# Kernel optimization log

Measured on AMD Instinct MI355X. Metric: run time of the kernel, lower is better.

The kernel has to match this reference:

```python
import jax, jax.numpy as jnp
import numpy as np

EPS = 1e-12
SIMILARITY = 'l2'


def setup_inputs() -> dict:
    key = jax.random.key(0)
    k1, k2, k3, k4 = jax.random.split(key, 4)
    N, M, D = 8192, 8192, 256
    x = jax.random.normal(k1, (N, D), dtype=jnp.float32)
    x_n = jax.random.normal(k2, (M, D), dtype=jnp.float32)
    W = jax.random.normal(k3, (D, 2), dtype=jnp.float32) / np.sqrt(D)
    b = jax.random.normal(k4, (2,), dtype=jnp.float32)
    return {"x": x, "x_n": x_n, "W": W, "b": b}


def _sim_matrix(x, x_n, similarity):
    if similarity == 'l2':
        x2 = jnp.sum(x * x, axis=1, keepdims=True)          # [N,1]
        xn2 = jnp.sum(x_n * x_n, axis=1, keepdims=True).T    # [1,M]
        d2 = jnp.maximum(x2 + xn2 - 2.0 * (x @ x_n.T), 0.0)
        return -jnp.sqrt(d2)
    elif similarity == 'l1':
        return -jnp.sum(jnp.abs(x[:, None, :] - x_n[None, :, :]), axis=-1)
    elif similarity == 'dot':
        return (x @ x_n.T) / x.shape[1]
    elif similarity == 'cos':
        xn_ = x / jnp.linalg.norm(x, axis=1, keepdims=True)
        xnn = x_n / jnp.linalg.norm(x_n, axis=1, keepdims=True)
        return xn_ @ xnn.T
    raise ValueError(similarity)


def reference(x, x_n, W, b) -> jnp.ndarray:
    # soft-KNN params from a small linear head
    params = jax.nn.sigmoid(x @ W + b)                      # [N,2]
    k = jnp.clip(params[:, 0:1], EPS, 1.0 - EPS)            # [N,1]
    t = jnp.clip(params[:, 1:2], EPS, 1.0 - EPS)            # [N,1]

    sim = _sim_matrix(x, x_n, SIMILARITY)                   # [N,M]
    sim_min = jnp.min(sim, axis=1, keepdims=True)
    sim_max = jnp.max(sim, axis=1, keepdims=True)
    sim = (sim - sim_min) / (sim_max - sim_min)             # row min-max normalize
    sim = jnp.maximum(sim, EPS)

    shift = t / (1.0 - t) * (k - sim) * jnp.log(sim / k)
    return sim + jnp.where(sim <= k, shift, 0.0)
```

## Files before the change

### kernel.cpp

```cpp
#include <hip/hip_runtime.h>
#include <hip/hip_bf16.h>
#include <cstdint>

#define N_ROWS 8192
#define M_ROWS 8192
#define DDIM   256
#define EPSF   1e-12f

typedef unsigned short u16;
typedef __attribute__((ext_vector_type(8))) short short8;
typedef __attribute__((ext_vector_type(4))) float floatx4;

__device__ inline void split_bf16(float v, u16& h, u16& lo) {
    __hip_bfloat16 hb = __float2bfloat16(v);
    float hf = __bfloat162float(hb);
    __hip_bfloat16 lb = __float2bfloat16(v - hf);
    h  = __builtin_bit_cast(u16, hb);
    lo = __builtin_bit_cast(u16, lb);
}

__global__ __launch_bounds__(256) void prep_x(
    const float* __restrict__ x, const float* __restrict__ W, const float* __restrict__ b,
    u16* __restrict__ xhi, u16* __restrict__ xlo,
    float* __restrict__ x2, float* __restrict__ karr, float* __restrict__ Carr,
    float* __restrict__ logkarr)
{
    const int l = threadIdx.x & 63;
    const int w = threadIdx.x >> 6;
    const int row = blockIdx.x * 4 + w;

    const float4 xv = *(const float4*)(x + (size_t)row * DDIM + l * 4);
    const float4 wa = *(const float4*)(W + l * 8);
    const float4 wb = *(const float4*)(W + l * 8 + 4);

    float s2 = xv.x * xv.x + xv.y * xv.y + xv.z * xv.z + xv.w * xv.w;
    float s0 = xv.x * wa.x + xv.y * wa.z + xv.z * wb.x + xv.w * wb.z;
    float s1 = xv.x * wa.y + xv.y * wa.w + xv.z * wb.y + xv.w * wb.w;

    u16 h0, l0, h1, l1, h2, l2, h3, l3;
    split_bf16(xv.x, h0, l0); split_bf16(xv.y, h1, l1);
    split_bf16(xv.z, h2, l2); split_bf16(xv.w, h3, l3);
    *(ushort4*)(xhi + (size_t)row * DDIM + l * 4) = make_ushort4(h0, h1, h2, h3);
    *(ushort4*)(xlo + (size_t)row * DDIM + l * 4) = make_ushort4(l0, l1, l2, l3);

    #pragma unroll
    for (int off = 32; off; off >>= 1) {
        s2 += __shfl_xor(s2, off);
        s0 += __shfl_xor(s0, off);
        s1 += __shfl_xor(s1, off);
    }
    if (l == 0) {
        float a0 = s0 + b[0];
        float a1 = s1 + b[1];
        float k = 1.0f / (1.0f + __expf(-a0));
        float t = 1.0f / (1.0f + __expf(-a1));
        k = fminf(fmaxf(k, EPSF), 1.0f - EPSF);
        t = fminf(fmaxf(t, EPSF), 1.0f - EPSF);
        x2[row] = s2;
        karr[row] = k;
        Carr[row] = t / (1.0f - t);
        logkarr[row] = logf(k);
    }
}

__global__ __launch_bounds__(256) void prep_xn(
    const float* __restrict__ xn,
    u16* __restrict__ xnhi, u16* __restrict__ xnlo, float* __restrict__ xn2)
{
    const int l = threadIdx.x & 63;
    const int w = threadIdx.x >> 6;
    const int row = blockIdx.x * 4 + w;

    const float4 xv = *(const float4*)(xn + (size_t)row * DDIM + l * 4);
    float s2 = xv.x * xv.x + xv.y * xv.y + xv.z * xv.z + xv.w * xv.w;

    u16 h0, l0, h1, l1, h2, l2, h3, l3;
    split_bf16(xv.x, h0, l0); split_bf16(xv.y, h1, l1);
    split_bf16(xv.z, h2, l2); split_bf16(xv.w, h3, l3);
    *(ushort4*)(xnhi + (size_t)row * DDIM + l * 4) = make_ushort4(h0, h1, h2, h3);
    *(ushort4*)(xnlo + (size_t)row * DDIM + l * 4) = make_ushort4(l0, l1, l2, l3);

    #pragma unroll
    for (int off = 32; off; off >>= 1) s2 += __shfl_xor(s2, off);
    if (l == 0) xn2[row] = s2;
}

__global__ __launch_bounds__(256) void gemm_s(
    const u16* __restrict__ xhi, const u16* __restrict__ xlo,
    const u16* __restrict__ xnhi, const u16* __restrict__ xnlo,
    const float* __restrict__ x2, const float* __restrict__ xn2,
    float* __restrict__ out)
{
    __shared__ u16 lds[16384];

    const int l  = threadIdx.x & 63;
    const int w  = threadIdx.x >> 6;
    const int wm = w >> 1;
    const int wn = w & 1;
    const int bRow = blockIdx.y;
    const int bCol = blockIdx.x;

    floatx4 acc[4][4];
    #pragma unroll
    for (int mi = 0; mi < 4; ++mi)
        #pragma unroll
        for (int ni = 0; ni < 4; ++ni)
            acc[mi][ni] = (floatx4){0.f, 0.f, 0.f, 0.f};

    const u16* bases[4] = {xhi, xlo, xnhi, xnlo};
    const int lrow = l & 15;
    const int lk8  = (l >> 4) * 8;

    for (int kk = 0; kk < DDIM / 32; ++kk) {
        const int ks = kk * 32;
        #pragma unroll
        for (int p = 0; p < 8; ++p) {
            const int id    = w * 8 + p;
            const int panel = id >> 3;
            const int tile  = id & 7;
            const int grow  = (panel < 2 ? bRow : bCol) * 128 + tile * 16 + lrow;
            const u16* src  = bases[panel] + (size_t)grow * DDIM + ks + lk8;
            u16* dst = &lds[panel * 4096 + tile * 512];
            __builtin_amdgcn_global_load_lds(
                (const __attribute__((address_space(1))) void*)src,
                (__attribute__((address_space(3))) void*)dst,
                16, 0, 0);
        }
        __syncthreads();

        short8 ah[4], al[4], bh[4], bl[4];
        #pragma unroll
        for (int i = 0; i < 4; ++i) {
            ah[i] = *(const short8*)&lds[0     + (wm * 4 + i) * 512 + l * 8];
            al[i] = *(const short8*)&lds[4096  + (wm * 4 + i) * 512 + l * 8];
            bh[i] = *(const short8*)&lds[8192  + (wn * 4 + i) * 512 + l * 8];
            bl[i] = *(const short8*)&lds[12288 + (wn * 4 + i) * 512 + l * 8];
        }
        #pragma unroll
        for (int mi = 0; mi < 4; ++mi)
            #pragma unroll
            for (int ni = 0; ni < 4; ++ni) {
                acc[mi][ni] = __builtin_amdgcn_mfma_f32_16x16x32_bf16(ah[mi], bh[ni], acc[mi][ni], 0, 0, 0);
                acc[mi][ni] = __builtin_amdgcn_mfma_f32_16x16x32_bf16(ah[mi], bl[ni], acc[mi][ni], 0, 0, 0);
                acc[mi][ni] = __builtin_amdgcn_mfma_f32_16x16x32_bf16(al[mi], bh[ni], acc[mi][ni], 0, 0, 0);
            }
        __syncthreads();
    }

    const int q  = l >> 4;
    const int cn = l & 15;
    #pragma unroll
    for (int mi = 0; mi < 4; ++mi) {
        #pragma unroll
        for (int r = 0; r < 4; ++r) {
            const int i = bRow * 128 + wm * 64 + mi * 16 + q * 4 + r;
            const float x2i = x2[i];
            #pragma unroll
            for (int ni = 0; ni < 4; ++ni) {
                const int j = bCol * 128 + wn * 64 + ni * 16 + cn;
                const float d2 = x2i + xn2[j] - 2.0f * acc[mi][ni][r];
                out[(size_t)i * M_ROWS + j] = -sqrtf(fmaxf(d2, 0.0f));
            }
        }
    }
}

__global__ __launch_bounds__(256) void transform_row(
    float* __restrict__ out, const float* __restrict__ x, const float* __restrict__ xn,
    const float* __restrict__ karr, const float* __restrict__ Carr,
    const float* __restrict__ logkarr)
{
    const int row = blockIdx.x;
    const int t = threadIdx.x;
    const int l = t & 63;
    const int w = t >> 6;

    __shared__ float wmin[4], wmax[4];
    __shared__ int cnt;
    __shared__ unsigned long long sMinBits;
    __shared__ int cidx[1024];
    __shared__ double cval[1024];

    const size_t rbase = (size_t)row * M_ROWS;
    float4 v[8];
    #pragma unroll
    for (int c = 0; c < 8; ++c)
        v[c] = *(const float4*)(out + rbase + c * 1024 + t * 4);

    float lmin = 1e30f, lmax = -1e30f;
    #pragma unroll
    for (int c = 0; c < 8; ++c) {
        lmin = fminf(lmin, fminf(fminf(v[c].x, v[c].y), fminf(v[c].z, v[c].w)));
        lmax = fmaxf(lmax, fmaxf(fmaxf(v[c].x, v[c].y), fmaxf(v[c].z, v[c].w)));
    }
    #pragma unroll
    for (int m = 1; m < 64; m <<= 1) {
        lmin = fminf(lmin, __shfl_xor(lmin, m));
        lmax = fmaxf(lmax, __shfl_xor(lmax, m));
    }
    if (l == 0) { wmin[w] = lmin; wmax[w] = lmax; }
    if (t == 0) { cnt = 0; sMinBits = 0ull; }
    __syncthreads();
    const float sminA = fminf(fminf(wmin[0], wmin[1]), fminf(wmin[2], wmin[3]));
    const float smaxA = fmaxf(fmaxf(wmax[0], wmax[1]), fmaxf(wmax[2], wmax[3]));
    const float thresh = sminA + 0.05f * (smaxA - sminA);

    int myPos[8], mySlot[8];
    int myCnt = 0;
    #pragma unroll
    for (int c = 0; c < 8; ++c) {
        const float* pv = (const float*)&v[c];
        #pragma unroll
        for (int u = 0; u < 4; ++u) {
            if (pv[u] <= thresh) {
                int pos = atomicAdd(&cnt, 1);
                if (pos < 1024 && myCnt < 8) {
                    cidx[pos] = c * 1024 + t * 4 + u;
                    myPos[myCnt] = pos;
                    mySlot[myCnt] = c * 4 + u;
                    myCnt++;
                }
            }
        }
    }
    __syncthreads();
    const int nc = min(cnt, 1024);

    const float4 xa = *(const float4*)(x + (size_t)row * DDIM + l * 4);
    const double dx0 = xa.x, dx1 = xa.y, dx2 = xa.z, dx3 = xa.w;
    double x2p = dx0 * dx0 + dx1 * dx1 + dx2 * dx2 + dx3 * dx3;
    #pragma unroll
    for (int m = 1; m < 64; m <<= 1) x2p += __shfl_xor(x2p, m);

    for (int c = w; c < nc; c += 4) {
        const int j = cidx[c];
        const float4 na = *(const float4*)(xn + (size_t)j * DDIM + l * 4);
        const double n0 = na.x, n1 = na.y, n2 = na.z, n3 = na.w;
        double dot = dx0 * n0 + dx1 * n1 + dx2 * n2 + dx3 * n3;
        double nn  = n0 * n0 + n1 * n1 + n2 * n2 + n3 * n3;
        #pragma unroll
        for (int m = 1; m < 64; m <<= 1) {
            dot += __shfl_xor(dot, m);
            nn  += __shfl_xor(nn, m);
        }
        if (l == 0) {
            double d2 = x2p + nn - 2.0 * dot;
            d2 = d2 > 0.0 ? d2 : 0.0;
            double se = -sqrt(d2);
            cval[c] = se;
            atomicMax(&sMinBits, (unsigned long long)__double_as_longlong(se));
        }
    }
    __syncthreads();

    const double sminD = __longlong_as_double((long long)sMinBits);
    const float k = karr[row], C = Carr[row], logk = logkarr[row];
    const float smin = (float)sminD;
    const double invD = 1.0 / ((double)smaxA - sminD);
    const float inv = (float)invD;

    float o[32];
    #pragma unroll
    for (int c = 0; c < 8; ++c) {
        const float* pv = (const float*)&v[c];
        #pragma unroll
        for (int u = 0; u < 4; ++u) {
            float sim = fmaxf((pv[u] - smin) * inv, EPSF);
            float r = sim;
            if (sim <= k) r += C * (k - sim) * (__logf(sim) - logk);
            o[c * 4 + u] = r;
        }
    }
    for (int q2 = 0; q2 < myCnt; ++q2) {
        double simd = (cval[myPos[q2]] - sminD) * invD;
        simd = simd > (double)EPSF ? simd : (double)EPSF;
        float sim = (float)simd;
        float r = sim;
        if (sim <= k) r += C * (k - sim) * (logf(sim) - logk);
        o[mySlot[q2]] = r;
    }
    #pragma unroll
    for (int c = 0; c < 8; ++c) {
        float4 ov;
        ov.x = o[c * 4 + 0]; ov.y = o[c * 4 + 1];
        ov.z = o[c * 4 + 2]; ov.w = o[c * 4 + 3];
        *(float4*)(out + rbase + c * 1024 + t * 4) = ov;
    }
}

extern "C" void kernel_launch(void* const* d_in, const int* in_sizes, int n_in,
                              void* d_out, int out_size, void* d_ws, size_t ws_size,
                              hipStream_t stream)
{
    const float* x  = (const float*)d_in[0];
    const float* xn = (const float*)d_in[1];
    const float* W  = (const float*)d_in[2];
    const float* b  = (const float*)d_in[3];
    float* out = (float*)d_out;

    uint8_t* ws = (uint8_t*)d_ws;
    u16* xhi  = (u16*)(ws);
    u16* xlo  = (u16*)(ws + (4u << 20));
    u16* xnhi = (u16*)(ws + (8u << 20));
    u16* xnlo = (u16*)(ws + (12u << 20));
    float* x2       = (float*)(ws + (16u << 20));
    float* xn2      = x2 + N_ROWS;
    float* karr     = xn2 + M_ROWS;
    float* Carr     = karr + N_ROWS;
    float* logkarr  = Carr + N_ROWS;

    prep_x<<<N_ROWS / 4, 256, 0, stream>>>(x, W, b, xhi, xlo, x2, karr, Carr, logkarr);
    prep_xn<<<M_ROWS / 4, 256, 0, stream>>>(xn, xnhi, xnlo, xn2);
    gemm_s<<<dim3(M_ROWS / 128, N_ROWS / 128), 256, 0, stream>>>(
        xhi, xlo, xnhi, xnlo, x2, xn2, out);
    transform_row<<<N_ROWS, 256, 0, stream>>>(out, x, xn, karr, Carr, logkarr);
}
```

Baseline: 519.2 us.

## Recompute single-bf16 GEMM twice to fuse transform and drop intermediate matrix

Replaces the 3-pass split-bf16 GEMM plus row-transform pass with two single-bf16 GEMM passes. The first pass only reduces per-row min/max distances via atomics, and the second recomputes the dot products and writes the final transformed output directly with nontemporal stores. Near-min candidates are collected into a global list, refined in double precision, and patched afterwards. This avoids writing and rereading the 256 MB similarity matrix and cuts MFMA work per pass, at the cost of a duplicated GEMM, lower bf16 accuracy elsewhere in each row, global atomic contention, and a capped candidate buffer.

New measurement: 1.166 ms. 124% more time.

```diff
diff --git a/kernel.cpp b/kernel.cpp
--- a/kernel.cpp
+++ b/kernel.cpp
@@ -6,24 +6,18 @@
 #define M_ROWS 8192
 #define DDIM   256
 #define EPSF   1e-12f
+#define CAND_CAP (1 << 18)
+#define THRESH_FRAC 0.08f
 
 typedef unsigned short u16;
+typedef unsigned long long u64;
 typedef __attribute__((ext_vector_type(8))) short short8;
 typedef __attribute__((ext_vector_type(4))) float floatx4;
 
-__device__ inline void split_bf16(float v, u16& h, u16& lo) {
-    __hip_bfloat16 hb = __float2bfloat16(v);
-    float hf = __bfloat162float(hb);
-    __hip_bfloat16 lb = __float2bfloat16(v - hf);
-    h  = __builtin_bit_cast(u16, hb);
-    lo = __builtin_bit_cast(u16, lb);
-}
-
 __global__ __launch_bounds__(256) void prep_x(
     const float* __restrict__ x, const float* __restrict__ W, const float* __restrict__ b,
-    u16* __restrict__ xhi, u16* __restrict__ xlo,
-    float* __restrict__ x2, float* __restrict__ karr, float* __restrict__ Carr,
-    float* __restrict__ logkarr)
+    u16* __restrict__ xhi, float* __restrict__ x2, float4* __restrict__ rowQ,
+    unsigned* __restrict__ rowD2MinU, unsigned* __restrict__ rowD2MaxU)
 {
     const int l = threadIdx.x & 63;
     const int w = threadIdx.x >> 6;
@@ -37,11 +31,12 @@
     float s0 = xv.x * wa.x + xv.y * wa.z + xv.z * wb.x + xv.w * wb.z;
     float s1 = xv.x * wa.y + xv.y * wa.w + xv.z * wb.y + xv.w * wb.w;
 
-    u16 h0, l0, h1, l1, h2, l2, h3, l3;
-    split_bf16(xv.x, h0, l0); split_bf16(xv.y, h1, l1);
-    split_bf16(xv.z, h2, l2); split_bf16(xv.w, h3, l3);
-    *(ushort4*)(xhi + (size_t)row * DDIM + l * 4) = make_ushort4(h0, h1, h2, h3);
-    *(ushort4*)(xlo + (size_t)row * DDIM + l * 4) = make_ushort4(l0, l1, l2, l3);
+    ushort4 hv;
+    hv.x = __builtin_bit_cast(u16, __float2bfloat16(xv.x));
+    hv.y = __builtin_bit_cast(u16, __float2bfloat16(xv.y));
+    hv.z = __builtin_bit_cast(u16, __float2bfloat16(xv.z));
+    hv.w = __builtin_bit_cast(u16, __float2bfloat16(xv.w));
+    *(ushort4*)(xhi + (size_t)row * DDIM + l * 4) = hv;
 
     #pragma unroll
     for (int off = 32; off; off >>= 1) {
@@ -57,15 +52,14 @@
         k = fminf(fmaxf(k, EPSF), 1.0f - EPSF);
         t = fminf(fmaxf(t, EPSF), 1.0f - EPSF);
         x2[row] = s2;
-        karr[row] = k;
-        Carr[row] = t / (1.0f - t);
-        logkarr[row] = logf(k);
+        rowQ[row] = make_float4(k, t / (1.0f - t), logf(k), 0.0f);
+        rowD2MinU[row] = 0x7F7FFFFFu;
+        rowD2MaxU[row] = 0u;
     }
 }
 
 __global__ __launch_bounds__(256) void prep_xn(
-    const float* __restrict__ xn,
-    u16* __restrict__ xnhi, u16* __restrict__ xnlo, float* __restrict__ xn2)
+    const float* __restrict__ xn, u16* __restrict__ xnhi, float* __restrict__ xn2)
 {
     const int l = threadIdx.x & 63;
     const int w = threadIdx.x >> 6;
@@ -74,25 +68,69 @@
     const float4 xv = *(const float4*)(xn + (size_t)row * DDIM + l * 4);
     float s2 = xv.x * xv.x + xv.y * xv.y + xv.z * xv.z + xv.w * xv.w;
 
-    u16 h0, l0, h1, l1, h2, l2, h3, l3;
-    split_bf16(xv.x, h0, l0); split_bf16(xv.y, h1, l1);
-    split_bf16(xv.z, h2, l2); split_bf16(xv.w, h3, l3);
-    *(ushort4*)(xnhi + (size_t)row * DDIM + l * 4) = make_ushort4(h0, h1, h2, h3);
-    *(ushort4*)(xnlo + (size_t)row * DDIM + l * 4) = make_ushort4(l0, l1, l2, l3);
+    ushort4 hv;
+    hv.x = __builtin_bit_cast(u16, __float2bfloat16(xv.x));
+    hv.y = __builtin_bit_cast(u16, __float2bfloat16(xv.y));
+    hv.z = __builtin_bit_cast(u16, __float2bfloat16(xv.z));
+    hv.w = __builtin_bit_cast(u16, __float2bfloat16(xv.w));
+    *(ushort4*)(xnhi + (size_t)row * DDIM + l * 4) = hv;
 
     #pragma unroll
     for (int off = 32; off; off >>= 1) s2 += __shfl_xor(s2, off);
     if (l == 0) xn2[row] = s2;
 }
 
-__global__ __launch_bounds__(256) void gemm_s(
-    const u16* __restrict__ xhi, const u16* __restrict__ xlo,
-    const u16* __restrict__ xnhi, const u16* __restrict__ xnlo,
+__device__ __forceinline__ void gemm_core(
+    const u16* __restrict__ xhi, const u16* __restrict__ xnhi,
+    u16* lds, int bRow, int bCol, int l, int w, int wm, int wn,
+    floatx4 acc[4][4])
+{
+    const int lrow = l & 15;
+    const int lk8  = (l >> 4) * 8;
+    #pragma unroll
+    for (int mi = 0; mi < 4; ++mi)
+        #pragma unroll
+        for (int ni = 0; ni < 4; ++ni)
+            acc[mi][ni] = (floatx4){0.f, 0.f, 0.f, 0.f};
+
+    for (int kk = 0; kk < DDIM / 32; ++kk) {
+        const int ks = kk * 32;
+        #pragma unroll
+        for (int p = 0; p < 4; ++p) {
+            const int id    = w * 4 + p;
+            const int panel = id >> 3;
+            const int tile  = id & 7;
+            const int grow  = (panel == 0 ? bRow : bCol) * 128 + tile * 16 + lrow;
+            const u16* src  = (panel == 0 ? xhi : xnhi) + (size_t)grow * DDIM + ks + lk8;
+            u16* dst = &lds[panel * 4096 + tile * 512];
+            __builtin_amdgcn_global_load_lds(
+                (const __attribute__((address_space(1))) void*)src,
+                (__attribute__((address_space(3))) void*)dst,
+                16, 0, 0);
+        }
+        __syncthreads();
+
+        short8 ah[4], bh[4];
+        #pragma unroll
+        for (int i = 0; i < 4; ++i) {
+            ah[i] = *(const short8*)&lds[0    + (wm * 4 + i) * 512 + l * 8];
+            bh[i] = *(const short8*)&lds[4096 + (wn * 4 + i) * 512 + l * 8];
+        }
+        #pragma unroll
+        for (int mi = 0; mi < 4; ++mi)
+            #pragma unroll
+            for (int ni = 0; ni < 4; ++ni)
+                acc[mi][ni] = __builtin_amdgcn_mfma_f32_16x16x32_bf16(ah[mi], bh[ni], acc[mi][ni], 0, 0, 0);
+        __syncthreads();
+    }
+}
+
+__global__ __launch_bounds__(256) void gemm_minmax(
+    const u16* __restrict__ xhi, const u16* __restrict__ xnhi,
     const float* __restrict__ x2, const float* __restrict__ xn2,
-    float* __restrict__ out)
-{
-    __shared__ u16 lds[16384];
-
+    unsigned* __restrict__ rowD2MinU, unsigned* __restrict__ rowD2MaxU)
+{
+    __shared__ u16 lds[8192];
     const int l  = threadIdx.x & 63;
     const int w  = threadIdx.x >> 6;
     const int wm = w >> 1;
@@ -101,51 +139,7 @@
     const int bCol = blockIdx.x;
 
     floatx4 acc[4][4];
-    #pragma unroll
-    for (int mi = 0; mi < 4; ++mi)
-        #pragma unroll
-        for (int ni = 0; ni < 4; ++ni)
-            acc[mi][ni] = (floatx4){0.f, 0.f, 0.f, 0.f};
-
-    const u16* bases[4] = {xhi, xlo, xnhi, xnlo};
-    const int lrow = l & 15;
-    const int lk8  = (l >> 4) * 8;
-
-    for (int kk = 0; kk < DDIM / 32; ++kk) {
-        const int ks = kk * 32;
-        #pragma unroll
-        for (int p = 0; p < 8; ++p) {
-            const int id    = w * 8 + p;
-            const int panel = id >> 3;
-            const int tile  = id & 7;
-            const int grow  = (panel < 2 ? bRow : bCol) * 128 + tile * 16 + lrow;
-            const u16* src  = bases[panel] + (size_t)grow * DDIM + ks + lk8;
-            u16* dst = &lds[panel * 4096 + tile * 512];
-            __builtin_amdgcn_global_load_lds(
-                (const __attribute__((address_space(1))) void*)src,
-                (__attribute__((address_space(3))) void*)dst,
-                16, 0, 0);
-        }
-        __syncthreads();
-
-        short8 ah[4], al[4], bh[4], bl[4];
-        #pragma unroll
-        for (int i = 0; i < 4; ++i) {
-            ah[i] = *(const short8*)&lds[0     + (wm * 4 + i) * 512 + l * 8];
-            al[i] = *(const short8*)&lds[4096  + (wm * 4 + i) * 512 + l * 8];
-            bh[i] = *(const short8*)&lds[8192  + (wn * 4 + i) * 512 + l * 8];
-            bl[i] = *(const short8*)&lds[12288 + (wn * 4 + i) * 512 + l * 8];
-        }
-        #pragma unroll
-        for (int mi = 0; mi < 4; ++mi)
-            #pragma unroll
-            for (int ni = 0; ni < 4; ++ni) {
-                acc[mi][ni] = __builtin_amdgcn_mfma_f32_16x16x32_bf16(ah[mi], bh[ni], acc[mi][ni], 0, 0, 0);
-                acc[mi][ni] = __builtin_amdgcn_mfma_f32_16x16x32_bf16(ah[mi], bl[ni], acc[mi][ni], 0, 0, 0);
-                acc[mi][ni] = __builtin_amdgcn_mfma_f32_16x16x32_bf16(al[mi], bh[ni], acc[mi][ni], 0, 0, 0);
-            }
-        __syncthreads();
-    }
+    gemm_core(xhi, xnhi, lds, bRow, bCol, l, w, wm, wn, acc);
 
     const int q  = l >> 4;
     const int cn = l & 15;
@@ -155,136 +149,144 @@
         for (int r = 0; r < 4; ++r) {
             const int i = bRow * 128 + wm * 64 + mi * 16 + q * 4 + r;
             const float x2i = x2[i];
+            float dmn = 3.0e38f, dmx = 0.0f;
             #pragma unroll
             for (int ni = 0; ni < 4; ++ni) {
                 const int j = bCol * 128 + wn * 64 + ni * 16 + cn;
-                const float d2 = x2i + xn2[j] - 2.0f * acc[mi][ni][r];
-                out[(size_t)i * M_ROWS + j] = -sqrtf(fmaxf(d2, 0.0f));
+                const float d2 = fmaxf(x2i + xn2[j] - 2.0f * acc[mi][ni][r], 0.0f);
+                dmn = fminf(dmn, d2);
+                dmx = fmaxf(dmx, d2);
             }
-        }
-    }
-}
-
-__global__ __launch_bounds__(256) void transform_row(
-    float* __restrict__ out, const float* __restrict__ x, const float* __restrict__ xn,
-    const float* __restrict__ karr, const float* __restrict__ Carr,
-    const float* __restrict__ logkarr)
-{
-    const int row = blockIdx.x;
-    const int t = threadIdx.x;
-    const int l = t & 63;
-    const int w = t >> 6;
-
-    __shared__ float wmin[4], wmax[4];
-    __shared__ int cnt;
-    __shared__ unsigned long long sMinBits;
-    __shared__ int cidx[1024];
-    __shared__ double cval[1024];
-
-    const size_t rbase = (size_t)row * M_ROWS;
-    float4 v[8];
-    #pragma unroll
-    for (int c = 0; c < 8; ++c)
-        v[c] = *(const float4*)(out + rbase + c * 1024 + t * 4);
-
-    float lmin = 1e30f, lmax = -1e30f;
-    #pragma unroll
-    for (int c = 0; c < 8; ++c) {
-        lmin = fminf(lmin, fminf(fminf(v[c].x, v[c].y), fminf(v[c].z, v[c].w)));
-        lmax = fmaxf(lmax, fmaxf(fmaxf(v[c].x, v[c].y), fmaxf(v[c].z, v[c].w)));
-    }
-    #pragma unroll
-    for (int m = 1; m < 64; m <<= 1) {
-        lmin = fminf(lmin, __shfl_xor(lmin, m));
-        lmax = fmaxf(lmax, __shfl_xor(lmax, m));
-    }
-    if (l == 0) { wmin[w] = lmin; wmax[w] = lmax; }
-    if (t == 0) { cnt = 0; sMinBits = 0ull; }
-    __syncthreads();
-    const float sminA = fminf(fminf(wmin[0], wmin[1]), fminf(wmin[2], wmin[3]));
-    const float smaxA = fmaxf(fmaxf(wmax[0], wmax[1]), fmaxf(wmax[2], wmax[3]));
-    const float thresh = sminA + 0.05f * (smaxA - sminA);
-
-    int myPos[8], mySlot[8];
-    int myCnt = 0;
-    #pragma unroll
-    for (int c = 0; c < 8; ++c) {
-        const float* pv = (const float*)&v[c];
-        #pragma unroll
-        for (int u = 0; u < 4; ++u) {
-            if (pv[u] <= thresh) {
-                int pos = atomicAdd(&cnt, 1);
-                if (pos < 1024 && myCnt < 8) {
-                    cidx[pos] = c * 1024 + t * 4 + u;
-                    myPos[myCnt] = pos;
-                    mySlot[myCnt] = c * 4 + u;
-                    myCnt++;
+            #pragma unroll
+            for (int m = 1; m < 16; m <<= 1) {
+                dmn = fminf(dmn, __shfl_xor(dmn, m));
+                dmx = fmaxf(dmx, __shfl_xor(dmx, m));
+            }
+            if (cn == 0) {
+                atomicMin(&rowD2MinU[i], __float_as_uint(dmn));
+                atomicMax(&rowD2MaxU[i], __float_as_uint(dmx));
+            }
+        }
+    }
+}
+
+__global__ __launch_bounds__(256) void rowfin(
+    const unsigned* __restrict__ rowD2MinU, const unsigned* __restrict__ rowD2MaxU,
+    float4* __restrict__ rowP, u64* __restrict__ rowMinBits, int* __restrict__ cntG)
+{
+    const int i = blockIdx.x * 256 + threadIdx.x;
+    const float smax = -sqrtf(__uint_as_float(rowD2MinU[i]));
+    const float smin = -sqrtf(__uint_as_float(rowD2MaxU[i]));
+    const float range = smax - smin;
+    rowP[i] = make_float4(smin, 1.0f / range, smin + THRESH_FRAC * range, smax);
+    rowMinBits[i] = 0ull;
+    if (i == 0) *cntG = 0;
+}
+
+__global__ __launch_bounds__(256) void gemm_out(
+    const u16* __restrict__ xhi, const u16* __restrict__ xnhi,
+    const float* __restrict__ x2, const float* __restrict__ xn2,
+    const float4* __restrict__ rowP, const float4* __restrict__ rowQ,
+    float* __restrict__ out, unsigned* __restrict__ cand, int* __restrict__ cntG)
+{
+    __shared__ u16 lds[8192];
+    const int l  = threadIdx.x & 63;
+    const int w  = threadIdx.x >> 6;
+    const int wm = w >> 1;
+    const int wn = w & 1;
+    const int bRow = blockIdx.y;
+    const int bCol = blockIdx.x;
+
+    floatx4 acc[4][4];
+    gemm_core(xhi, xnhi, lds, bRow, bCol, l, w, wm, wn, acc);
+
+    const int q  = l >> 4;
+    const int cn = l & 15;
+    #pragma unroll
+    for (int mi = 0; mi < 4; ++mi) {
+        #pragma unroll
+        for (int r = 0; r < 4; ++r) {
+            const int i = bRow * 128 + wm * 64 + mi * 16 + q * 4 + r;
+            const float x2i  = x2[i];
+            const float4 P = rowP[i];
+            const float4 Q = rowQ[i];
+            #pragma unroll
+            for (int ni = 0; ni < 4; ++ni) {
+                const int j = bCol * 128 + wn * 64 + ni * 16 + cn;
+                const float d2 = fmaxf(x2i + xn2[j] - 2.0f * acc[mi][ni][r], 0.0f);
+                const float s = -sqrtf(d2);
+                if (s <= P.z) {
+                    int pos = atomicAdd(cntG, 1);
+                    if (pos < CAND_CAP) cand[pos] = ((unsigned)i << 13) | (unsigned)j;
                 }
+                float sim = fmaxf((s - P.x) * P.y, EPSF);
+                float rv = sim;
+                if (sim <= Q.x) rv += Q.y * (Q.x - sim) * (__logf(sim) - Q.z);
+                __builtin_nontemporal_store(rv, &out[(size_t)i * M_ROWS + j]);
             }
         }
     }
-    __syncthreads();
-    const int nc = min(cnt, 1024);
-
-    const float4 xa = *(const float4*)(x + (size_t)row * DDIM + l * 4);
-    const double dx0 = xa.x, dx1 = xa.y, dx2 = xa.z, dx3 = xa.w;
-    double x2p = dx0 * dx0 + dx1 * dx1 + dx2 * dx2 + dx3 * dx3;
-    #pragma unroll
-    for (int m = 1; m < 64; m <<= 1) x2p += __shfl_xor(x2p, m);
-
-    for (int c = w; c < nc; c += 4) {
-        const int j = cidx[c];
-        const float4 na = *(const float4*)(xn + (size_t)j * DDIM + l * 4);
-        const double n0 = na.x, n1 = na.y, n2 = na.z, n3 = na.w;
-        double dot = dx0 * n0 + dx1 * n1 + dx2 * n2 + dx3 * n3;
-        double nn  = n0 * n0 + n1 * n1 + n2 * n2 + n3 * n3;
+}
+
+__global__ __launch_bounds__(256) void refine(
+    const float* __restrict__ x, const float* __restrict__ xn,
+    const unsigned* __restrict__ cand, const int* __restrict__ cntG,
+    double* __restrict__ cexact, u64* __restrict__ rowMinBits)
+{
+    const int l = threadIdx.x & 63;
+    const int w = threadIdx.x >> 6;
+    const int gw = blockIdx.x * 4 + w;
+    const int nwaves = gridDim.x * 4;
+    const int nc = min(*cntG, CAND_CAP);
+
+    for (int c = gw; c < nc; c += nwaves) {
+        const unsigned rc = cand[c];
+        const int row = rc >> 13;
+        const int col = rc & 8191;
+        const float4 xa = *(const float4*)(x  + (size_t)row * DDIM + l * 4);
+        const float4 na = *(const float4*)(xn + (size_t)col * DDIM + l * 4);
+        const double x0 = xa.x, x1 = xa.y, x2v = xa.z, x3 = xa.w;
+        const double n0 = na.x, n1 = na.y, n2v = na.z, n3 = na.w;
+        double xx  = x0 * x0 + x1 * x1 + x2v * x2v + x3 * x3;
+        double nn  = n0 * n0 + n1 * n1 + n2v * n2v + n3 * n3;
+        double dot = x0 * n0 + x1 * n1 + x2v * n2v + x3 * n3;
         #pragma unroll
         for (int m = 1; m < 64; m <<= 1) {
+            xx  += __shfl_xor(xx, m);
+            nn  += __shfl_xor(nn, m);
             dot += __shfl_xor(dot, m);
-            nn  += __shfl_xor(nn, m);
         }
         if (l == 0) {
-            double d2 = x2p + nn - 2.0 * dot;
+            double d2 = xx + nn - 2.0 * dot;
             d2 = d2 > 0.0 ? d2 : 0.0;
-            double se = -sqrt(d2);
-            cval[c] = se;
-            atomicMax(&sMinBits, (unsigned long long)__double_as_longlong(se));
-        }
-    }
-    __syncthreads();
-
-    const double sminD = __longlong_as_double((long long)sMinBits);
-    const float k = karr[row], C = Carr[row], logk = logkarr[row];
-    const float smin = (float)sminD;
-    const double invD = 1.0 / ((double)smaxA - sminD);
-    const float inv = (float)invD;
-
-    float o[32];
-    #pragma unroll
-    for (int c = 0; c < 8; ++c) {
-        const float* pv = (const float*)&v[c];
-        #pragma unroll
-        for (int u = 0; u < 4; ++u) {
-            float sim = fmaxf((pv[u] - smin) * inv, EPSF);
-            float r = sim;
-            if (sim <= k) r += C * (k - sim) * (__logf(sim) - logk);
-            o[c * 4 + u] = r;
-        }
-    }
-    for (int q2 = 0; q2 < myCnt; ++q2) {
-        double simd = (cval[myPos[q2]] - sminD) * invD;
+            const double se = -sqrt(d2);
+            cexact[c] = se;
+            atomicMax(&rowMinBits[row], (u64)__double_as_longlong(se));
+        }
+    }
+}
+
+__global__ __launch_bounds__(256) void patch(
+    const unsigned* __restrict__ cand, const int* __restrict__ cntG,
+    const double* __restrict__ cexact, const u64* __restrict__ rowMinBits,
+    const float4* __restrict__ rowP, const float4* __restrict__ rowQ,
+    float* __restrict__ out)
+{
+    const int nc = min(*cntG, CAND_CAP);
+    for (int c = blockIdx.x * 256 + threadIdx.x; c < nc; c += gridDim.x * 256) {
+        const unsigned rc = cand[c];
+        const int row = rc >> 13;
+        const int col = rc & 8191;
+        const double se = cexact[c];
+        const double sminD = __longlong_as_double((long long)rowMinBits[row]);
+        const double invD = 1.0 / ((double)rowP[row].w - sminD);
+        double simd = (se - sminD) * invD;
         simd = simd > (double)EPSF ? simd : (double)EPSF;
-        float sim = (float)simd;
-        float r = sim;
-        if (sim <= k) r += C * (k - sim) * (logf(sim) - logk);
-        o[mySlot[q2]] = r;
-    }
-    #pragma unroll
-    for (int c = 0; c < 8; ++c) {
-        float4 ov;
-        ov.x = o[c * 4 + 0]; ov.y = o[c * 4 + 1];
-        ov.z = o[c * 4 + 2]; ov.w = o[c * 4 + 3];
-        *(float4*)(out + rbase + c * 1024 + t * 4) = ov;
+        const float sim = (float)simd;
+        const float4 Q = rowQ[row];
+        float rv = sim;
+        if (sim <= Q.x) rv += Q.y * (Q.x - sim) * (logf(sim) - Q.z);
+        out[(size_t)row * M_ROWS + col] = rv;
     }
 }
 
@@ -299,19 +301,26 @@
     float* out = (float*)d_out;
 
     uint8_t* ws = (uint8_t*)d_ws;
-    u16* xhi  = (u16*)(ws);
-    u16* xlo  = (u16*)(ws + (4u << 20));
-    u16* xnhi = (u16*)(ws + (8u << 20));
-    u16* xnlo = (u16*)(ws + (12u << 20));
-    float* x2       = (float*)(ws + (16u << 20));
-    float* xn2      = x2 + N_ROWS;
-    float* karr     = xn2 + M_ROWS;
-    float* Carr     = karr + N_ROWS;
-    float* logkarr  = Carr + N_ROWS;
-
-    prep_x<<<N_ROWS / 4, 256, 0, stream>>>(x, W, b, xhi, xlo, x2, karr, Carr, logkarr);
-    prep_xn<<<M_ROWS / 4, 256, 0, stream>>>(xn, xnhi, xnlo, xn2);
-    gemm_s<<<dim3(M_ROWS / 128, N_ROWS / 128), 256, 0, stream>>>(
-        xhi, xlo, xnhi, xnlo, x2, xn2, out);
-    transform_row<<<N_ROWS, 256, 0, stream>>>(out, x, xn, karr, Carr, logkarr);
-}
+    u16* xhi   = (u16*)(ws);
+    u16* xnhi  = (u16*)(ws + (4u << 20));
+    float* x2  = (float*)(ws + (8u << 20));
+    float* xn2 = x2 + N_ROWS;
+    float4* rowQ = (float4*)(xn2 + M_ROWS);
+    float4* rowP = rowQ + N_ROWS;
+    unsigned* rowD2MinU = (unsigned*)(rowP + N_ROWS);
+    unsigned* rowD2MaxU = rowD2MinU + N_ROWS;
+    u64* rowMinBits = (u64*)(rowD2MaxU + N_ROWS);
+    int* cntG = (int*)(rowMinBits + N_ROWS);
+    unsigned* cand = (unsigned*)((uint8_t*)cntG + 16);
+    double* cexact = (double*)((uint8_t*)cand + (size_t)CAND_CAP * 4);
+
+    prep_x<<<N_ROWS / 4, 256, 0, stream>>>(x, W, b, xhi, x2, rowQ, rowD2MinU, rowD2MaxU);
+    prep_xn<<<M_ROWS / 4, 256, 0, stream>>>(xn, xnhi, xn2);
+    gemm_minmax<<<dim3(M_ROWS / 128, N_ROWS / 128), 256, 0, stream>>>(
+        xhi, xnhi, x2, xn2, rowD2MinU, rowD2MaxU);
+    rowfin<<<N_ROWS / 256, 256, 0, stream>>>(rowD2MinU, rowD2MaxU, rowP, rowMinBits, cntG);
+    gemm_out<<<dim3(M_ROWS / 128, N_ROWS / 128), 256, 0, stream>>>(
+        xhi, xnhi, x2, xn2, rowP, rowQ, out, cand, cntG);
+    refine<<<512, 256, 0, stream>>>(x, xn, cand, cntG, cexact, rowMinBits);
+    patch<<<256, 256, 0, stream>>>(cand, cntG, cexact, rowMinBits, rowP, rowQ, out);
+}
```
